# Kernel optimization log

Hardware: AMD Instinct MI355X
Metric: run time of the kernel (lower is better)

Reference implementation:

```python
import jax, jax.numpy as jnp
import numpy as np

VOCAB_SIZE = 4096
D_EMBED = 256
BETA = 0.25  # unused: module returns raw commit_loss; beta applied by caller


def setup_inputs() -> dict:
    key = jax.random.key(0)
    k_h, k_e = jax.random.split(key)
    h = jax.random.normal(k_h, (16, D_EMBED, 32, 32), dtype=jnp.float32)
    embedding = jax.random.normal(k_e, (VOCAB_SIZE, D_EMBED), dtype=jnp.float32)
    return {"h": h, "embedding": embedding}


def reference(h, embedding):
    B, C, H, W = h.shape
    h = h.astype(jnp.float32)
    # (B, C, H, W) -> (N, C) with N = B*H*W
    h_flat = jnp.transpose(h, (0, 2, 3, 1)).reshape(-1, C)
    dist = (
        jnp.sum(h_flat * h_flat, axis=1, keepdims=True)
        + jnp.sum(embedding * embedding, axis=1)
        - 2.0 * jnp.einsum("nc,vc->nv", h_flat, embedding)
    )
    indices_flat = jnp.argmin(dist, axis=1)
    indices = indices_flat.reshape(B, H, W)
    # gather codebook vectors and restore (B, C, H, W)
    z_q = jnp.transpose(embedding[indices_flat].reshape(B, H, W, C), (0, 3, 1, 2))
    commit_loss = jnp.mean((h - jax.lax.stop_gradient(z_q)) ** 2)
    # straight-through estimator
    z_q_st = h + jax.lax.stop_gradient(z_q - h)
    return z_q_st, indices, commit_loss
```

## Files before the change

kernel.cpp:

```cpp
#include <hip/hip_runtime.h>

#define D 256
#define VOCAB 4096
#define NTOT 16384
#define N_OUT0 4194304

typedef _Float16 half8 __attribute__((ext_vector_type(8)));
typedef float f32x4 __attribute__((ext_vector_type(4)));

__device__ __forceinline__ void gld16(const void* g, void* l) {
    __builtin_amdgcn_global_load_lds(
        (const __attribute__((address_space(1))) void*)g,
        (__attribute__((address_space(3))) void*)l, 16, 0, 0);
}

__device__ __forceinline__ unsigned long long pack_key(float d, int v) {
    unsigned u = __float_as_uint(d);
    u ^= ((unsigned)((int)u >> 31)) | 0x80000000u;
    return ((unsigned long long)u << 32) | (unsigned)v;
}

__global__ __launch_bounds__(64) void k_prep(const float* __restrict__ emb,
                                             float* __restrict__ esq,
                                             unsigned long long* __restrict__ gbest,
                                             float* __restrict__ out2) {
    const int v = blockIdx.x, lane = threadIdx.x;
    float4 e = *(const float4*)(emb + (size_t)v * D + lane * 4);
    float s = e.x * e.x + e.y * e.y + e.z * e.z + e.w * e.w;
#pragma unroll
    for (int m = 32; m >= 1; m >>= 1) s += __shfl_xor(s, m, 64);
    if (lane == 0) esq[v] = s;
    if (v < NTOT / 64) gbest[(size_t)v * 64 + lane] = ~0ULL;
    if (v == 0 && lane == 0) out2[0] = 0.0f;
}

__global__ __launch_bounds__(256) void k_pack(const float* __restrict__ h,
                                              const float* __restrict__ emb,
                                              _Float16* __restrict__ Apk,
                                              _Float16* __restrict__ Bpk) {
    __shared__ float S[8192];
    const int tid = threadIdx.x;
    const int bid = blockIdx.x;
    if (bid < 512) {
        const int bm = bid >> 3, w = bid & 7;
        const int b = bm >> 2, p0 = (bm & 3) * 256;
        const float* src = h + ((size_t)b << 18) + p0;
#pragma unroll 4
        for (int cl = 0; cl < 32; ++cl)
            S[cl * 256 + tid] = src[(size_t)(w * 32 + cl) << 10 | (unsigned)tid];
        __syncthreads();
        _Float16* dstT = Apk + (size_t)bm * 131072 + (size_t)w * 16384;
#pragma unroll
        for (int i = 0; i < 4; ++i) {
            alignas(16) _Float16 hi[8], lo[8];
#pragma unroll
            for (int j = 0; j < 8; ++j) {
                float vv = S[(i * 8 + j) * 256 + tid];
                _Float16 hv = (_Float16)vv;
                hi[j] = hv;
                lo[j] = (_Float16)(vv - (float)hv);
            }
            _Float16* dst = dstT + i * 2048 + tid * 8;
            *(half8*)dst = *(half8*)hi;
            *(half8*)(dst + 8192) = *(half8*)lo;
        }
    } else {
        const int bid2 = bid - 512;
        const int bn = bid2 >> 3, w = bid2 & 7;
        const int v0 = bn * 128;
#pragma unroll 4
        for (int i = 0; i < 16; ++i) {
            int flat = i * 256 + tid;
            int r = flat >> 5, cl = flat & 31;
            S[cl * 129 + r] = emb[(size_t)(v0 + r) * D + w * 32 + cl];
        }
        __syncthreads();
        _Float16* dstT = Bpk + (size_t)bn * 65536 + (size_t)w * 8192;
#pragma unroll
        for (int i = 0; i < 2; ++i) {
            int s = i * 256 + tid;
            int q = s >> 7, r = s & 127;
            alignas(16) _Float16 hi[8], lo[8];
#pragma unroll
            for (int j = 0; j < 8; ++j) {
                float vv = S[(q * 8 + j) * 129 + r];
                _Float16 hv = (_Float16)vv;
                hi[j] = hv;
                lo[j] = (_Float16)(vv - (float)hv);
            }
            _Float16* dst = dstT + q * 1024 + r * 8;
            *(half8*)dst = *(half8*)hi;
            *(half8*)(dst + 4096) = *(half8*)lo;
        }
    }
}

__global__ __launch_bounds__(256, 2) void k_gemm(const _Float16* __restrict__ Apk,
                                                 const _Float16* __restrict__ Bpk,
                                                 const float* __restrict__ esq,
                                                 unsigned long long* __restrict__ gbest) {
    __shared__ _Float16 As[16384];
    __shared__ _Float16 Bs[8192];
    __shared__ unsigned long long red[256];

    const int tid = threadIdx.x;
    const int bm = blockIdx.x >> 5, bn = blockIdx.x & 31;
    const int m0 = bm * 256, n0 = bn * 128;
    red[tid] = ~0ULL;

    const int wv = tid >> 6, l = tid & 63;
    const int wm = wv & 1, wn = wv >> 1;
    const int quad = l >> 4, j16 = l & 15;

    f32x4 acc[8][4];
#pragma unroll
    for (int i = 0; i < 8; ++i)
#pragma unroll
        for (int j = 0; j < 4; ++j) acc[i][j] = (f32x4)0.0f;

    const _Float16* Aw0 = Apk + (size_t)bm * 131072;
    const _Float16* Bw0 = Bpk + (size_t)bn * 65536;
    const _Float16* aBase = As + quad * 2048 + (wm * 128 + j16) * 8;
    const _Float16* bBase = Bs + quad * 1024 + (wn * 64 + j16) * 8;

    for (int w = 0; w < 8; ++w) {
        const _Float16* Aw = Aw0 + w * 16384;
        const _Float16* Bw = Bw0 + w * 8192;
#pragma unroll
        for (int i = 0; i < 8; ++i) gld16(Aw + i * 2048 + tid * 8, As + i * 2048 + tid * 8);
#pragma unroll
        for (int i = 0; i < 4; ++i) gld16(Bw + i * 2048 + tid * 8, Bs + i * 2048 + tid * 8);
        __syncthreads();

        half8 af[8], bf[4];
#pragma unroll
        for (int mt = 0; mt < 8; ++mt) af[mt] = *(const half8*)(aBase + mt * 128);
#pragma unroll
        for (int nt = 0; nt < 4; ++nt) bf[nt] = *(const half8*)(bBase + 4096 + nt * 128);
#pragma unroll
        for (int mt = 0; mt < 8; ++mt)
#pragma unroll
            for (int nt = 0; nt < 4; ++nt)
                acc[mt][nt] = __builtin_amdgcn_mfma_f32_16x16x32_f16(af[mt], bf[nt], acc[mt][nt], 0, 0, 0);
#pragma unroll
        for (int nt = 0; nt < 4; ++nt) bf[nt] = *(const half8*)(bBase + nt * 128);
#pragma unroll
        for (int mt = 0; mt < 8; ++mt)
#pragma unroll
            for (int nt = 0; nt < 4; ++nt)
                acc[mt][nt] = __builtin_amdgcn_mfma_f32_16x16x32_f16(af[mt], bf[nt], acc[mt][nt], 0, 0, 0);
#pragma unroll
        for (int mt = 0; mt < 8; ++mt) af[mt] = *(const half8*)(aBase + 8192 + mt * 128);
#pragma unroll
        for (int mt = 0; mt < 8; ++mt)
#pragma unroll
            for (int nt = 0; nt < 4; ++nt)
                acc[mt][nt] = __builtin_amdgcn_mfma_f32_16x16x32_f16(af[mt], bf[nt], acc[mt][nt], 0, 0, 0);
        __syncthreads();
    }

    float es[4];
#pragma unroll
    for (int nt = 0; nt < 4; ++nt) es[nt] = esq[n0 + wn * 64 + nt * 16 + j16];
#pragma unroll
    for (int mt = 0; mt < 8; ++mt) {
#pragma unroll
        for (int r = 0; r < 4; ++r) {
            unsigned long long best = ~0ULL;
#pragma unroll
            for (int nt = 0; nt < 4; ++nt) {
                float dv = es[nt] - 2.0f * acc[mt][nt][r];
                unsigned long long key = pack_key(dv, n0 + wn * 64 + nt * 16 + j16);
                best = key < best ? key : best;
            }
#pragma unroll
            for (int m = 8; m >= 1; m >>= 1) {
                unsigned long long o = __shfl_xor(best, m, 64);
                best = o < best ? o : best;
            }
            if (j16 == 0) atomicMin(&red[wm * 128 + mt * 16 + quad * 4 + r], best);
        }
    }
    __syncthreads();
    atomicMin(&gbest[m0 + tid], red[tid]);
}

__global__ __launch_bounds__(256) void k_gather(const float* __restrict__ h,
                                                const float* __restrict__ emb,
                                                const unsigned long long* __restrict__ gbest,
                                                float* __restrict__ out0,
                                                float* __restrict__ out1,
                                                float* __restrict__ out2) {
    __shared__ float zq[32][260];
    __shared__ float wred[4];
    const int tid = threadIdx.x;
    const int lane = tid & 63;
    const int w = tid >> 6;
    const int n0 = blockIdx.x * 32;
    const int b = n0 >> 10;
    const int p0 = n0 & 1023;
#pragma unroll
    for (int rr = 0; rr < 8; ++rr) {
        int r = w * 8 + rr;
        unsigned idx = (unsigned)(gbest[n0 + r] & 0xFFFFFFFFULL);
        float4 e4 = *(const float4*)(emb + (size_t)idx * D + lane * 4);
        *(float4*)&zq[r][lane * 4] = e4;
    }
    if (tid < 32) {
        unsigned idx = (unsigned)(gbest[n0 + tid] & 0xFFFFFFFFULL);
        out1[n0 + tid] = (float)idx;
    }
    __syncthreads();
    float lsum = 0.0f;
    const size_t base = ((size_t)b * D) << 10;
#pragma unroll 4
    for (int it = 0; it < 32; ++it) {
        int c = it * 8 + (tid >> 5);
        int pp = tid & 31;
        float z = zq[pp][c];
        size_t g = base + ((size_t)c << 10) + p0 + pp;
        float hv = h[g];
        out0[g] = hv + (z - hv);
        float d = hv - z;
        lsum = fmaf(d, d, lsum);
    }
#pragma unroll
    for (int m = 32; m >= 1; m >>= 1) lsum += __shfl_xor(lsum, m, 64);
    if (lane == 0) wred[w] = lsum;
    __syncthreads();
    if (tid == 0)
        atomicAdd(out2, (wred[0] + wred[1] + wred[2] + wred[3]) * (1.0f / (float)N_OUT0));
}

extern "C" void kernel_launch(void* const* d_in, const int* in_sizes, int n_in,
                              void* d_out, int out_size, void* d_ws, size_t ws_size,
                              hipStream_t stream) {
    const float* h = (const float*)d_in[0];
    const float* emb = (const float*)d_in[1];
    float* out0 = (float*)d_out;
    float* out1 = out0 + N_OUT0;
    float* out2 = out1 + NTOT;

    _Float16* Apk = (_Float16*)d_ws;
    _Float16* Bpk = (_Float16*)((char*)d_ws + 16777216);
    float* esq = (float*)((char*)d_ws + 16777216 + 4194304);
    unsigned long long* gbest = (unsigned long long*)((char*)d_ws + 16777216 + 4194304 + 16384);

    hipLaunchKernelGGL(k_prep, dim3(VOCAB), dim3(64), 0, stream, emb, esq, gbest, out2);
    hipLaunchKernelGGL(k_pack, dim3(768), dim3(256), 0, stream, h, emb, Apk, Bpk);
    hipLaunchKernelGGL(k_gemm, dim3(2048), dim3(256), 0, stream, Apk, Bpk, esq, gbest);
    hipLaunchKernelGGL(k_gather, dim3(NTOT / 32), dim3(256), 0, stream, h, emb, gbest, out0, out1, out2);
}
```

Baseline: 201.7 us.

## Replace split-fp16 GEMM with single fp16 pass plus fp32 candidate refinement

Drops the hi/lo fp16 split (three MFMA passes) for a single fp16 GEMM that records each row's top-2 keys per 128-column tile. A reduce kernel uses an error bound derived from the row norm to pick candidates that could be the true argmin. A refine kernel then recomputes those candidates exactly in fp32. This cuts tensor-core work and pack traffic by about two thirds, but adds two kernels, an atomic job queue, and a dependence on the error bound and job capacity being large enough to stay correct.

```diff
diff --git a/kernel.cpp b/kernel.cpp
--- a/kernel.cpp
+++ b/kernel.cpp
@@ -4,6 +4,7 @@
 #define VOCAB 4096
 #define NTOT 16384
 #define N_OUT0 4194304
+#define JOB_CAP 262144
 
 typedef _Float16 half8 __attribute__((ext_vector_type(8)));
 typedef float f32x4 __attribute__((ext_vector_type(4)));
@@ -20,94 +21,103 @@
     return ((unsigned long long)u << 32) | (unsigned)v;
 }
 
-__global__ __launch_bounds__(64) void k_prep(const float* __restrict__ emb,
-                                             float* __restrict__ esq,
-                                             unsigned long long* __restrict__ gbest,
-                                             float* __restrict__ out2) {
-    const int v = blockIdx.x, lane = threadIdx.x;
-    float4 e = *(const float4*)(emb + (size_t)v * D + lane * 4);
-    float s = e.x * e.x + e.y * e.y + e.z * e.z + e.w * e.w;
-#pragma unroll
-    for (int m = 32; m >= 1; m >>= 1) s += __shfl_xor(s, m, 64);
-    if (lane == 0) esq[v] = s;
-    if (v < NTOT / 64) gbest[(size_t)v * 64 + lane] = ~0ULL;
-    if (v == 0 && lane == 0) out2[0] = 0.0f;
+__device__ __forceinline__ float unkey(unsigned long long k) {
+    unsigned u = (unsigned)(k >> 32);
+    u = (u & 0x80000000u) ? (u ^ 0x80000000u) : ~u;
+    return __uint_as_float(u);
+}
+
+__device__ __forceinline__ void pmerge(unsigned long long& k1, unsigned long long& k2,
+                                       unsigned long long o1, unsigned long long o2) {
+    unsigned long long lo = o1 < k1 ? o1 : k1;
+    unsigned long long hi = o1 < k1 ? k1 : o1;
+    unsigned long long s2 = o2 < k2 ? o2 : k2;
+    k1 = lo;
+    k2 = hi < s2 ? hi : s2;
 }
 
 __global__ __launch_bounds__(256) void k_pack(const float* __restrict__ h,
                                               const float* __restrict__ emb,
                                               _Float16* __restrict__ Apk,
-                                              _Float16* __restrict__ Bpk) {
-    __shared__ float S[8192];
+                                              _Float16* __restrict__ Bpk,
+                                              float* __restrict__ esq,
+                                              float* __restrict__ hsq,
+                                              unsigned long long* __restrict__ gbest,
+                                              unsigned int* __restrict__ jobcnt,
+                                              float* __restrict__ out2) {
+    __shared__ float S[16384];
     const int tid = threadIdx.x;
     const int bid = blockIdx.x;
-    if (bid < 512) {
-        const int bm = bid >> 3, w = bid & 7;
-        const int b = bm >> 2, p0 = (bm & 3) * 256;
-        const float* src = h + ((size_t)b << 18) + p0;
-#pragma unroll 4
-        for (int cl = 0; cl < 32; ++cl)
-            S[cl * 256 + tid] = src[(size_t)(w * 32 + cl) << 10 | (unsigned)tid];
-        __syncthreads();
-        _Float16* dstT = Apk + (size_t)bm * 131072 + (size_t)w * 16384;
-#pragma unroll
-        for (int i = 0; i < 4; ++i) {
-            alignas(16) _Float16 hi[8], lo[8];
-#pragma unroll
-            for (int j = 0; j < 8; ++j) {
-                float vv = S[(i * 8 + j) * 256 + tid];
-                _Float16 hv = (_Float16)vv;
-                hi[j] = hv;
-                lo[j] = (_Float16)(vv - (float)hv);
-            }
-            _Float16* dst = dstT + i * 2048 + tid * 8;
-            *(half8*)dst = *(half8*)hi;
-            *(half8*)(dst + 8192) = *(half8*)lo;
-        }
+    if (bid < 64) {
+        const int bm = bid;
+        const int b = bm >> 2, p0 = (bm & 3) << 8;
+        float hacc = 0.f;
+        _Float16* dstA = Apk + (size_t)bm * 65536;
+        for (int w = 0; w < 4; ++w) {
+            __syncthreads();
+#pragma unroll 4
+            for (int cl = 0; cl < 64; ++cl)
+                S[cl * 256 + tid] =
+                    h[((size_t)b << 18) + ((size_t)(w * 64 + cl) << 10) + (size_t)(p0 + tid)];
+            __syncthreads();
+#pragma unroll 4
+            for (int cl = 0; cl < 64; ++cl) { float x = S[cl * 256 + tid]; hacc = fmaf(x, x, hacc); }
+#pragma unroll
+            for (int kk = 0; kk < 2; ++kk)
+#pragma unroll
+                for (int q = 0; q < 4; ++q) {
+                    alignas(16) _Float16 hv[8];
+#pragma unroll
+                    for (int j = 0; j < 8; ++j) hv[j] = (_Float16)S[(kk * 32 + q * 8 + j) * 256 + tid];
+                    *(half8*)(dstA + w * 16384 + (kk * 4 + q) * 2048 + tid * 8) = *(half8*)hv;
+                }
+        }
+        hsq[(bm << 8) + tid] = hacc;
+    } else if (bid < 96) {
+        const int bn = bid - 64, v0 = bn << 7;
+        float eacc = 0.f;
+        _Float16* dstB = Bpk + (size_t)bn * 32768;
+        const int kk = tid >> 7, r = tid & 127;
+        for (int w = 0; w < 4; ++w) {
+            __syncthreads();
+#pragma unroll 4
+            for (int i = 0; i < 32; ++i) {
+                int rr = i * 4 + (tid >> 6), cc = tid & 63;
+                S[rr * 65 + cc] = emb[(size_t)(v0 + rr) * 256 + w * 64 + cc];
+            }
+            __syncthreads();
+            if (tid < 128)
+#pragma unroll 4
+                for (int cc = 0; cc < 64; ++cc) { float x = S[tid * 65 + cc]; eacc = fmaf(x, x, eacc); }
+#pragma unroll
+            for (int q = 0; q < 4; ++q) {
+                alignas(16) _Float16 ev[8];
+#pragma unroll
+                for (int j = 0; j < 8; ++j) ev[j] = (_Float16)S[r * 65 + kk * 32 + q * 8 + j];
+                *(half8*)(dstB + w * 8192 + (kk * 4 + q) * 1024 + r * 8) = *(half8*)ev;
+            }
+        }
+        if (tid < 128) esq[v0 + tid] = eacc;
     } else {
-        const int bid2 = bid - 512;
-        const int bn = bid2 >> 3, w = bid2 & 7;
-        const int v0 = bn * 128;
-#pragma unroll 4
-        for (int i = 0; i < 16; ++i) {
-            int flat = i * 256 + tid;
-            int r = flat >> 5, cl = flat & 31;
-            S[cl * 129 + r] = emb[(size_t)(v0 + r) * D + w * 32 + cl];
-        }
-        __syncthreads();
-        _Float16* dstT = Bpk + (size_t)bn * 65536 + (size_t)w * 8192;
-#pragma unroll
-        for (int i = 0; i < 2; ++i) {
-            int s = i * 256 + tid;
-            int q = s >> 7, r = s & 127;
-            alignas(16) _Float16 hi[8], lo[8];
-#pragma unroll
-            for (int j = 0; j < 8; ++j) {
-                float vv = S[(q * 8 + j) * 129 + r];
-                _Float16 hv = (_Float16)vv;
-                hi[j] = hv;
-                lo[j] = (_Float16)(vv - (float)hv);
-            }
-            _Float16* dst = dstT + q * 1024 + r * 8;
-            *(half8*)dst = *(half8*)hi;
-            *(half8*)(dst + 4096) = *(half8*)lo;
-        }
+        const int base = (bid - 96) * 2048;
+#pragma unroll
+        for (int r2 = 0; r2 < 8; ++r2) gbest[base + r2 * 256 + tid] = ~0ULL;
+        if (bid == 96 && tid == 0) { *jobcnt = 0u; *out2 = 0.f; }
     }
 }
 
 __global__ __launch_bounds__(256, 2) void k_gemm(const _Float16* __restrict__ Apk,
                                                  const _Float16* __restrict__ Bpk,
                                                  const float* __restrict__ esq,
-                                                 unsigned long long* __restrict__ gbest) {
+                                                 unsigned long long* __restrict__ top2) {
     __shared__ _Float16 As[16384];
     __shared__ _Float16 Bs[8192];
-    __shared__ unsigned long long red[256];
-
-    const int tid = threadIdx.x;
-    const int bm = blockIdx.x >> 5, bn = blockIdx.x & 31;
-    const int m0 = bm * 256, n0 = bn * 128;
-    red[tid] = ~0ULL;
-
+    __shared__ unsigned long long redA[256][2];
+    __shared__ unsigned long long redB[256][2];
+
+    const int tid = threadIdx.x;
+    const int bn = blockIdx.x >> 6, bm = blockIdx.x & 63;
+    const int m0 = bm << 8, n0 = bn << 7;
     const int wv = tid >> 6, l = tid & 63;
     const int wm = wv & 1, wn = wv >> 1;
     const int quad = l >> 4, j16 = l & 15;
@@ -118,71 +128,164 @@
 #pragma unroll
         for (int j = 0; j < 4; ++j) acc[i][j] = (f32x4)0.0f;
 
-    const _Float16* Aw0 = Apk + (size_t)bm * 131072;
-    const _Float16* Bw0 = Bpk + (size_t)bn * 65536;
-    const _Float16* aBase = As + quad * 2048 + (wm * 128 + j16) * 8;
-    const _Float16* bBase = Bs + quad * 1024 + (wn * 64 + j16) * 8;
-
-    for (int w = 0; w < 8; ++w) {
-        const _Float16* Aw = Aw0 + w * 16384;
-        const _Float16* Bw = Bw0 + w * 8192;
-#pragma unroll
-        for (int i = 0; i < 8; ++i) gld16(Aw + i * 2048 + tid * 8, As + i * 2048 + tid * 8);
-#pragma unroll
-        for (int i = 0; i < 4; ++i) gld16(Bw + i * 2048 + tid * 8, Bs + i * 2048 + tid * 8);
+    const char* Ag = (const char*)(Apk + (size_t)bm * 65536) + tid * 16;
+    const char* Bg = (const char*)(Bpk + (size_t)bn * 32768) + tid * 16;
+    _Float16* Asw = As + tid * 8;
+    _Float16* Bsw = Bs + tid * 8;
+    const _Float16* aB = As + quad * 2048 + (wm * 128 + j16) * 8;
+    const _Float16* bB = Bs + quad * 1024 + (wn * 64 + j16) * 8;
+
+    for (int w = 0; w < 4; ++w) {
+#pragma unroll
+        for (int i = 0; i < 8; ++i) gld16(Ag + w * 32768 + i * 4096, Asw + i * 2048);
+#pragma unroll
+        for (int i = 0; i < 4; ++i) gld16(Bg + w * 16384 + i * 4096, Bsw + i * 2048);
         __syncthreads();
-
-        half8 af[8], bf[4];
-#pragma unroll
-        for (int mt = 0; mt < 8; ++mt) af[mt] = *(const half8*)(aBase + mt * 128);
-#pragma unroll
-        for (int nt = 0; nt < 4; ++nt) bf[nt] = *(const half8*)(bBase + 4096 + nt * 128);
-#pragma unroll
-        for (int mt = 0; mt < 8; ++mt)
-#pragma unroll
-            for (int nt = 0; nt < 4; ++nt)
-                acc[mt][nt] = __builtin_amdgcn_mfma_f32_16x16x32_f16(af[mt], bf[nt], acc[mt][nt], 0, 0, 0);
-#pragma unroll
-        for (int nt = 0; nt < 4; ++nt) bf[nt] = *(const half8*)(bBase + nt * 128);
-#pragma unroll
-        for (int mt = 0; mt < 8; ++mt)
-#pragma unroll
-            for (int nt = 0; nt < 4; ++nt)
-                acc[mt][nt] = __builtin_amdgcn_mfma_f32_16x16x32_f16(af[mt], bf[nt], acc[mt][nt], 0, 0, 0);
-#pragma unroll
-        for (int mt = 0; mt < 8; ++mt) af[mt] = *(const half8*)(aBase + 8192 + mt * 128);
-#pragma unroll
-        for (int mt = 0; mt < 8; ++mt)
-#pragma unroll
-            for (int nt = 0; nt < 4; ++nt)
-                acc[mt][nt] = __builtin_amdgcn_mfma_f32_16x16x32_f16(af[mt], bf[nt], acc[mt][nt], 0, 0, 0);
+#pragma unroll
+        for (int kk = 0; kk < 2; ++kk) {
+            half8 af[8], bf[4];
+#pragma unroll
+            for (int mt = 0; mt < 8; ++mt) af[mt] = *(const half8*)(aB + kk * 8192 + mt * 128);
+#pragma unroll
+            for (int nt = 0; nt < 4; ++nt) bf[nt] = *(const half8*)(bB + kk * 4096 + nt * 128);
+#pragma unroll
+            for (int mt = 0; mt < 8; ++mt)
+#pragma unroll
+                for (int nt = 0; nt < 4; ++nt)
+                    acc[mt][nt] = __builtin_amdgcn_mfma_f32_16x16x32_f16(af[mt], bf[nt], acc[mt][nt], 0, 0, 0);
+        }
         __syncthreads();
     }
 
-    float es[4];
-#pragma unroll
-    for (int nt = 0; nt < 4; ++nt) es[nt] = esq[n0 + wn * 64 + nt * 16 + j16];
+    float es4[4];
+#pragma unroll
+    for (int nt = 0; nt < 4; ++nt) es4[nt] = esq[n0 + wn * 64 + nt * 16 + j16];
 #pragma unroll
     for (int mt = 0; mt < 8; ++mt) {
 #pragma unroll
         for (int r = 0; r < 4; ++r) {
-            unsigned long long best = ~0ULL;
+            unsigned long long k1 = ~0ULL, k2 = ~0ULL;
 #pragma unroll
             for (int nt = 0; nt < 4; ++nt) {
-                float dv = es[nt] - 2.0f * acc[mt][nt][r];
-                unsigned long long key = pack_key(dv, n0 + wn * 64 + nt * 16 + j16);
-                best = key < best ? key : best;
-            }
-#pragma unroll
-            for (int m = 8; m >= 1; m >>= 1) {
+                float dv = es4[nt] - 2.0f * acc[mt][nt][r];
+                pmerge(k1, k2, pack_key(dv, n0 + wn * 64 + nt * 16 + j16), ~0ULL);
+            }
+#pragma unroll
+            for (int m = 1; m <= 8; m <<= 1) {
+                unsigned long long o1 = __shfl_xor(k1, m, 64);
+                unsigned long long o2 = __shfl_xor(k2, m, 64);
+                pmerge(k1, k2, o1, o2);
+            }
+            if (j16 == 0) {
+                int row = wm * 128 + mt * 16 + quad * 4 + r;
+                if (wn == 0) { redA[row][0] = k1; redA[row][1] = k2; }
+                else         { redB[row][0] = k1; redB[row][1] = k2; }
+            }
+        }
+    }
+    __syncthreads();
+    {
+        unsigned long long a1 = redA[tid][0], a2 = redA[tid][1];
+        unsigned long long b1 = redB[tid][0], b2 = redB[tid][1];
+        unsigned long long n1 = a1 < b1 ? a1 : b1;
+        unsigned long long hi = a1 < b1 ? b1 : a1;
+        unsigned long long s2 = a2 < b2 ? a2 : b2;
+        unsigned long long n2 = hi < s2 ? hi : s2;
+        size_t o = ((size_t)(m0 + tid) << 6) | ((unsigned)bn << 1);
+        top2[o] = n1;
+        top2[o | 1] = n2;
+    }
+}
+
+__global__ __launch_bounds__(256) void k_reduce(const unsigned long long* __restrict__ top2,
+                                                const float* __restrict__ hsq,
+                                                unsigned int* __restrict__ jobcnt,
+                                                unsigned int* __restrict__ jobs) {
+    const int tid = threadIdx.x;
+    const int n = blockIdx.x * 4 + (tid >> 6);
+    const int lane = tid & 63;
+    unsigned long long key = top2[((size_t)n << 6) | (unsigned)lane];
+    unsigned long long m1 = key;
+#pragma unroll
+    for (int m = 32; m >= 1; m >>= 1) {
+        unsigned long long o = __shfl_xor(m1, m, 64);
+        m1 = o < m1 ? o : m1;
+    }
+    float m1f = unkey(m1);
+    float Bn = 0.0215f * sqrtf(hsq[n]) + 0.02f;
+    float thr = m1f + 2.0f * Bn;
+    float df = unkey(key);
+    if (df <= thr) {
+        unsigned int job;
+        if ((lane & 1) == 0)
+            job = ((unsigned)n << 12) | (unsigned)(key & 0xFFFULL);
+        else
+            job = 0x80000000u | ((unsigned)n << 5) | (unsigned)(lane >> 1);
+        unsigned pos = atomicAdd(jobcnt, 1u);
+        if (pos < JOB_CAP) jobs[pos] = job;
+    }
+}
+
+__global__ __launch_bounds__(256) void k_refine(const float* __restrict__ h,
+                                                const float* __restrict__ emb,
+                                                const float* __restrict__ esq,
+                                                const unsigned int* __restrict__ jobcnt,
+                                                const unsigned int* __restrict__ jobs,
+                                                unsigned long long* __restrict__ gbest) {
+    const int tid = threadIdx.x;
+    const int l = tid & 63, wv = tid >> 6;
+    unsigned cnt = *jobcnt;
+    if (cnt > JOB_CAP) cnt = JOB_CAP;
+    unsigned j = blockIdx.x * 4 + wv;
+    const unsigned stride = gridDim.x * 4;
+    for (; j < cnt; j += stride) {
+        const unsigned job = jobs[j];
+        if (job & 0x80000000u) {
+            const int n = (int)((job >> 5) & 0x3FFFu);
+            const int bn = (int)(job & 31u);
+            const int b = n >> 10, p = n & 1023;
+            float hreg[4];
+#pragma unroll
+            for (int i = 0; i < 4; ++i)
+                hreg[i] = h[((size_t)b << 18) + ((size_t)(l * 4 + i) << 10) + (size_t)p];
+            const int vv0 = (bn << 7) + l, vv1 = vv0 + 64;
+            float a0 = 0.f, a1 = 0.f;
+            for (int k4 = 0; k4 < 64; ++k4) {
+                float4 e0 = *(const float4*)(emb + ((size_t)vv0 << 8) + k4 * 4);
+                float4 e1 = *(const float4*)(emb + ((size_t)vv1 << 8) + k4 * 4);
+                float h0 = __shfl(hreg[0], k4, 64);
+                float h1 = __shfl(hreg[1], k4, 64);
+                float h2 = __shfl(hreg[2], k4, 64);
+                float h3 = __shfl(hreg[3], k4, 64);
+                a0 = fmaf(h0, e0.x, a0); a0 = fmaf(h1, e0.y, a0);
+                a0 = fmaf(h2, e0.z, a0); a0 = fmaf(h3, e0.w, a0);
+                a1 = fmaf(h0, e1.x, a1); a1 = fmaf(h1, e1.y, a1);
+                a1 = fmaf(h2, e1.z, a1); a1 = fmaf(h3, e1.w, a1);
+            }
+            unsigned long long k0 = pack_key(esq[vv0] - 2.0f * a0, vv0);
+            unsigned long long k1 = pack_key(esq[vv1] - 2.0f * a1, vv1);
+            unsigned long long best = k0 < k1 ? k0 : k1;
+#pragma unroll
+            for (int m = 32; m >= 1; m >>= 1) {
                 unsigned long long o = __shfl_xor(best, m, 64);
                 best = o < best ? o : best;
             }
-            if (j16 == 0) atomicMin(&red[wm * 128 + mt * 16 + quad * 4 + r], best);
-        }
-    }
-    __syncthreads();
-    atomicMin(&gbest[m0 + tid], red[tid]);
+            if (l == 0) atomicMin(&gbest[n], best);
+        } else {
+            const int n = (int)(job >> 12);
+            const int v = (int)(job & 0xFFFu);
+            const int b = n >> 10, p = n & 1023;
+            float4 e4 = *(const float4*)(emb + ((size_t)v << 8) + l * 4);
+            float part = 0.f;
+            part = fmaf(h[((size_t)b << 18) + ((size_t)(l * 4 + 0) << 10) + p], e4.x, part);
+            part = fmaf(h[((size_t)b << 18) + ((size_t)(l * 4 + 1) << 10) + p], e4.y, part);
+            part = fmaf(h[((size_t)b << 18) + ((size_t)(l * 4 + 2) << 10) + p], e4.z, part);
+            part = fmaf(h[((size_t)b << 18) + ((size_t)(l * 4 + 3) << 10) + p], e4.w, part);
+#pragma unroll
+            for (int m = 32; m >= 1; m >>= 1) part += __shfl_xor(part, m, 64);
+            if (l == 0) atomicMin(&gbest[n], pack_key(esq[v] - 2.0f * part, v));
+        }
+    }
 }
 
 __global__ __launch_bounds__(256) void k_gather(const float* __restrict__ h,
@@ -241,13 +344,19 @@
     float* out1 = out0 + N_OUT0;
     float* out2 = out1 + NTOT;
 
-    _Float16* Apk = (_Float16*)d_ws;
-    _Float16* Bpk = (_Float16*)((char*)d_ws + 16777216);
-    float* esq = (float*)((char*)d_ws + 16777216 + 4194304);
-    unsigned long long* gbest = (unsigned long long*)((char*)d_ws + 16777216 + 4194304 + 16384);
-
-    hipLaunchKernelGGL(k_prep, dim3(VOCAB), dim3(64), 0, stream, emb, esq, gbest, out2);
-    hipLaunchKernelGGL(k_pack, dim3(768), dim3(256), 0, stream, h, emb, Apk, Bpk);
-    hipLaunchKernelGGL(k_gemm, dim3(2048), dim3(256), 0, stream, Apk, Bpk, esq, gbest);
+    char* w = (char*)d_ws;
+    _Float16* Apk = (_Float16*)(w);
+    _Float16* Bpk = (_Float16*)(w + 8388608);
+    unsigned long long* top2 = (unsigned long long*)(w + 10485760);
+    float* esq = (float*)(w + 18874368);
+    float* hsq = (float*)(w + 18890752);
+    unsigned long long* gbest = (unsigned long long*)(w + 18956288);
+    unsigned int* jobs = (unsigned int*)(w + 19087360);
+    unsigned int* jobcnt = (unsigned int*)(w + 20135936);
+
+    hipLaunchKernelGGL(k_pack, dim3(104), dim3(256), 0, stream, h, emb, Apk, Bpk, esq, hsq, gbest, jobcnt, out2);
+    hipLaunchKernelGGL(k_gemm, dim3(2048), dim3(256), 0, stream, Apk, Bpk, esq, top2);
+    hipLaunchKernelGGL(k_reduce, dim3(4096), dim3(256), 0, stream, top2, hsq, jobcnt, jobs);
+    hipLaunchKernelGGL(k_refine, dim3(512), dim3(256), 0, stream, h, emb, esq, jobcnt, jobs, gbest);
     hipLaunchKernelGGL(k_gather, dim3(NTOT / 32), dim3(256), 0, stream, h, emb, gbest, out0, out1, out2);
 }
```

Result: slower. 418.0 us (+107.3%).
